# Optimization experiments

Measured on AMD Instinct MI355X. Metric: run time of the kernel, lower is better.

The kernel has to match this reference:

```python
import jax, jax.numpy as jnp
import numpy as np

B, L, D = 32, 256, 128


def hard_sigmoid(x):
    # Keras-1 default inner_activation for LSTM gates
    return jnp.clip(0.2 * x + 0.5, 0.0, 1.0)


def lstm_step(x_t, h, c, W, U, b):
    # Keras-1 gate order: i, f, c(candidate), o
    z = x_t @ W + h @ U + b  # [B, 4D]
    d = h.shape[-1]
    i = hard_sigmoid(z[:, :d])
    f = hard_sigmoid(z[:, d:2 * d])
    g = jnp.tanh(z[:, 2 * d:3 * d])
    o = hard_sigmoid(z[:, 3 * d:])
    c_new = f * c + i * g
    h_new = o * jnp.tanh(c_new)
    return h_new, c_new


def setup_inputs() -> dict:
    key = jax.random.key(0)
    ks = jax.random.split(key, 9)
    s = 0.05  # weight scale to keep activations in a sane range
    return {
        "x": jax.random.normal(ks[0], (B, L, D), dtype=jnp.float32),
        "Wr": jax.random.normal(ks[1], (D, 4 * D), dtype=jnp.float32) * s,
        "Ur": jax.random.normal(ks[2], (D, 4 * D), dtype=jnp.float32) * s,
        "br": jnp.zeros((4 * D,), dtype=jnp.float32),
        "Ww": jax.random.normal(ks[3], (D, 4 * D), dtype=jnp.float32) * s,
        "Uw": jax.random.normal(ks[4], (D, 4 * D), dtype=jnp.float32) * s,
        "bw": jnp.zeros((4 * D,), dtype=jnp.float32),
        "Wc": jax.random.normal(ks[5], (2 * D, D), dtype=jnp.float32) * s,
        "bc": jnp.zeros((D,), dtype=jnp.float32),
    }


def reference(x, Wr, Ur, br, Ww, Uw, bw, Wc, bc):
    b, l, d = x.shape
    h0 = jnp.zeros((b, d), dtype=x.dtype)

    # ---- reader LSTM (return_sequences) ----
    def reader_step(carry, x_t):
        h, c = carry
        h, c = lstm_step(x_t, h, c, Wr, Ur, br)
        return (h, c), h

    _, o_seq = jax.lax.scan(reader_step, (h0, h0), jnp.swapaxes(x, 0, 1))  # [L, B, D]

    # ---- compose-and-write scan over timesteps ----
    mem0 = x  # read() sets mem_0 = input

    def write_step(carry, o_t):
        mem, h, c = carry  # mem: [B, L, D]
        # eq 2-3: attention over memory slots
        z = jax.nn.softmax(jnp.einsum('bd,bld->bl', o_t, mem), axis=-1)  # [B, L]
        m_rt = jnp.einsum('bl,bld->bd', z, mem)  # [B, D]
        # eq 4: composer (linear activation)
        c_t = jnp.concatenate([o_t, m_rt], axis=-1) @ Wc + bc  # [B, D]
        # eq 5: writer LSTM step
        h, c = lstm_step(c_t, h, c, Ww, Uw, bw)
        # eq 6: soft overwrite of memory
        zc = z[:, :, None]
        mem = mem * (1.0 - zc) + h[:, None, :] * zc
        return (mem, h, c), h

    (_, _, _), hs = jax.lax.scan(write_step, (mem0, h0, h0), o_seq)
    # return_mode == 'last_output'
    return hs[-1]
```

## Files before the change

### kernel.cpp

```cpp
#include <hip/hip_runtime.h>
#include <stdint.h>


#define LL 256

typedef float v2f __attribute__((ext_vector_type(2)));

__device__ __forceinline__ float hsig(float x) { return fminf(fmaxf(fmaf(x, 0.2f, 0.5f), 0.f), 1.f); }
__device__ __forceinline__ float tanh_fast(float x) {
  x = fminf(fmaxf(x, -15.f), 15.f);
  float e = __expf(2.f * x);
  return (e - 1.f) / (e + 1.f);
}

__global__ __launch_bounds__(512) void wtrans_kernel(const float* __restrict__ src,
                                                     float* __restrict__ dst, int jshift) {
  int idx = blockIdx.x * 512 + threadIdx.x;
  int J = 1 << jshift;
  int k = idx >> jshift, j = idx & (J - 1);
  dst[(((size_t)(k >> 2) << jshift) + j) * 4 + (k & 3)] = src[idx];
}

__global__ __launch_bounds__(512) void pvw_gemm(const float* __restrict__ Wc,
                                                const float* __restrict__ Ww,
                                                float* __restrict__ PVw) {
  __shared__ float wrow[128];
  const int r = blockIdx.x, j = threadIdx.x;
  if (j < 128) wrow[j] = Wc[r * 128 + j];
  __syncthreads();
  float a = 0.f;
#pragma unroll 4
  for (int m = 0; m < 128; m++) a = fmaf(wrow[m], Ww[m * 512 + j], a);
  PVw[r * 512 + j] = a;
}

__global__ __launch_bounds__(512) void pz_kernel(const float* __restrict__ bc,
                                                 const float* __restrict__ Ww,
                                                 const float* __restrict__ bw,
                                                 float* __restrict__ pz) {
  __shared__ float b_s[128];
  const int j = threadIdx.x;
  if (j < 128) b_s[j] = bc[j];
  __syncthreads();
  float a = bw[j];
#pragma unroll 4
  for (int m = 0; m < 128; m++) a = fmaf(b_s[m], Ww[m * 512 + j], a);
  pz[j] = a;
}

__global__ __launch_bounds__(512) void xw_gemm(const float* __restrict__ x,
                                               const float4* __restrict__ WrT4,
                                               const float* __restrict__ br,
                                               float* __restrict__ XW) {
  alignas(16) __shared__ float xs[8][128];
  const int b = blockIdx.x >> 5, tg = blockIdx.x & 31, tid = threadIdx.x;
  const float* xg = x + ((size_t)b * LL + tg * 8) * 128;
  if (tid < 256) ((float4*)&xs[0][0])[tid] = ((const float4*)xg)[tid];
  __syncthreads();
  float acc[8];
#pragma unroll
  for (int r = 0; r < 8; r++) acc[r] = 0.f;
#pragma unroll 8
  for (int i4 = 0; i4 < 32; i4++) {
    float4 w4 = WrT4[i4 * 512 + tid];
#pragma unroll
    for (int r = 0; r < 8; r++) {
      float4 v = *(const float4*)&xs[r][4 * i4];
      acc[r] += w4.x * v.x + w4.y * v.y + w4.z * v.z + w4.w * v.w;
    }
  }
  const float brj = br[tid];
  float* o = XW + ((size_t)b * LL + tg * 8) * 512;
#pragma unroll
  for (int r = 0; r < 8; r++) o[r * 512 + tid] = acc[r] + brj;
}

__global__ __launch_bounds__(512, 2) void reader_kernel(const float4* __restrict__ UrT4,
                                                        const float* __restrict__ XW,
                                                        float* __restrict__ og) {
  alignas(16) __shared__ float h_s[128];
  alignas(16) __shared__ float pp_s[512];
  const int b = blockIdx.x, tid = threadIdx.x;
  const float* XWb = XW + (size_t)b * LL * 512;
  float* ogb = og + (size_t)b * LL * 128;

  float4 U[32];
#pragma unroll
  for (int i4 = 0; i4 < 32; i4++) U[i4] = UrT4[i4 * 512 + tid];

  float c_r = 0.f;
  if (tid < 128) h_s[tid] = 0.f;
  float xwv = XWb[tid];
  __syncthreads();

  for (int t = 0; t < LL; t++) {
    float xw_n = (t + 1 < LL) ? XWb[(t + 1) * 512 + tid] : 0.f;
    v2f acc[4] = {{0.f, 0.f}, {0.f, 0.f}, {0.f, 0.f}, {0.f, 0.f}};
#pragma unroll
    for (int i4 = 0; i4 < 32; i4++) {
      float4 v = *(const float4*)&h_s[4 * i4];
      float4 w = U[i4];
      acc[i4 & 3] += (v2f){w.x, w.y} * (v2f){v.x, v.y};
      acc[i4 & 3] += (v2f){w.z, w.w} * (v2f){v.z, v.w};
    }
    v2f A = (acc[0] + acc[1]) + (acc[2] + acc[3]);
    pp_s[tid] = A.x + A.y + xwv;
    __syncthreads();
    if (tid < 128) {
      float zi = pp_s[tid], zf = pp_s[128 + tid], zg = pp_s[256 + tid], zo = pp_s[384 + tid];
      float ii = hsig(zi), ff = hsig(zf), gg = tanh_fast(zg), oo = hsig(zo);
      c_r = fmaf(ff, c_r, ii * gg);
      float h = oo * tanh_fast(c_r);
      h_s[tid] = h;
      ogb[t * 128 + tid] = h;
    }
    __syncthreads();
    xwv = xw_n;
  }
}

__global__ __launch_bounds__(512, 2) void writer_kernel(
    const float* __restrict__ x,
    const float4* __restrict__ VwT4, const float4* __restrict__ UwT4,
    const float* __restrict__ og, const float* __restrict__ ZW,
    float* __restrict__ out, const int NC) {
  alignas(16) __shared__ float h_s[128];
  alignas(16) __shared__ float osN[128];
  alignas(16) __shared__ float sc_s[256], ee_s[256];
  alignas(16) __shared__ float mr_s[128];
  alignas(16) __shared__ float pp_s[1024];
  __shared__ float rr_s[16];
  extern __shared__ float4 UwL[];

  const int b = blockIdx.x, tid = threadIdx.x;
  const int lane = tid & 63, wv = tid >> 6;
  const int l = tid >> 1, hf = tid & 1;
  const int q = tid >> 6, dp = tid & 63;

  const float* xg = x + (size_t)b * (LL * 128);
  const float* ogb = og + (size_t)b * (LL * 128);
  const float* ZWb = ZW + (size_t)b * (LL * 512);

  for (int i = tid; i < NC * 512; i += 512) UwL[i] = UwT4[i];

  v2f Mr[32], Mc[32];
#pragma unroll
  for (int w = 0; w < 32; w++) Mr[w] = *(const v2f*)(xg + l * 128 + hf * 64 + 2 * w);
#pragma unroll
  for (int i = 0; i < 32; i++) Mc[i] = *(const v2f*)(xg + (q * 32 + i) * 128 + 2 * dp);

  float c_w = 0.f;
  if (tid < 128) { h_s[tid] = 0.f; osN[tid] = ogb[tid]; }
  __syncthreads();
  {
    v2f S = {0.f, 0.f};
#pragma unroll
    for (int w = 0; w < 32; w++) S += Mr[w] * (*(const v2f*)&osN[hf * 64 + 2 * w]);
    float s = S.x + S.y;
    s += __shfl_xor(s, 1);
    if (hf == 0) sc_s[l] = s;
  }
  __syncthreads();

  for (int t = 0; t < LL; t++) {
    float zwv = ZWb[(size_t)t * 512 + tid];
    if (tid >= 128 && tid < 256 && t + 1 < LL)
      osN[tid - 128] = ogb[(t + 1) * 128 + (tid - 128)];
    if (tid < 256) {
      float m = sc_s[tid];
#pragma unroll
      for (int off = 32; off > 0; off >>= 1) m = fmaxf(m, __shfl_xor(m, off));
      if (lane == 0) rr_s[wv] = m;
    }
    __syncthreads();
    if (tid < 256) {
      float mx = fmaxf(fmaxf(rr_s[0], rr_s[1]), fmaxf(rr_s[2], rr_s[3]));
      float e = __expf(sc_s[tid] - mx);
      ee_s[tid] = e;
      float s2 = e;
#pragma unroll
      for (int off = 32; off > 0; off >>= 1) s2 += __shfl_xor(s2, off);
      if (lane == 0) rr_s[8 + wv] = s2;
    }
    __syncthreads();
    const float inv = 1.f / (rr_s[8] + rr_s[9] + rr_s[10] + rr_s[11]);
    {
      v2f P = {0.f, 0.f};
#pragma unroll
      for (int i = 0; i < 32; i++) P += Mc[i] * ee_s[q * 32 + i];
      *(v2f*)&pp_s[q * 128 + 2 * dp] = P;
    }
    __syncthreads();
    if (tid < 128) {
      float s = 0.f;
#pragma unroll
      for (int g = 0; g < 8; g++) s += pp_s[g * 128 + tid];
      mr_s[tid] = s * inv;
    }
    __syncthreads();
    {
      v2f a0 = {0.f, 0.f}, a1 = {0.f, 0.f}, a2 = {0.f, 0.f}, a3 = {0.f, 0.f};
#pragma unroll 2
      for (int i4 = 0; i4 < 32; i4 += 2) {
        float4 w0 = VwT4[i4 * 512 + tid];
        float4 w1 = VwT4[(i4 + 1) * 512 + tid];
        float4 v0 = *(const float4*)&mr_s[4 * i4];
        float4 v1 = *(const float4*)&mr_s[4 * i4 + 4];
        a0 += (v2f){w0.x, w0.y} * (v2f){v0.x, v0.y};
        a0 += (v2f){w0.z, w0.w} * (v2f){v0.z, v0.w};
        a1 += (v2f){w1.x, w1.y} * (v2f){v1.x, v1.y};
        a1 += (v2f){w1.z, w1.w} * (v2f){v1.z, v1.w};
      }
#pragma unroll 2
      for (int i4 = 0; i4 < NC; i4 += 2) {
        float4 w0 = UwL[i4 * 512 + tid];
        float4 w1 = UwL[(i4 + 1) * 512 + tid];
        float4 v0 = *(const float4*)&h_s[4 * i4];
        float4 v1 = *(const float4*)&h_s[4 * i4 + 4];
        a2 += (v2f){w0.x, w0.y} * (v2f){v0.x, v0.y};
        a2 += (v2f){w0.z, w0.w} * (v2f){v0.z, v0.w};
        a3 += (v2f){w1.x, w1.y} * (v2f){v1.x, v1.y};
        a3 += (v2f){w1.z, w1.w} * (v2f){v1.z, v1.w};
      }
#pragma unroll 2
      for (int i4 = NC; i4 < 32; i4 += 2) {
        float4 w0 = UwT4[i4 * 512 + tid];
        float4 w1 = UwT4[(i4 + 1) * 512 + tid];
        float4 v0 = *(const float4*)&h_s[4 * i4];
        float4 v1 = *(const float4*)&h_s[4 * i4 + 4];
        a0 += (v2f){w0.x, w0.y} * (v2f){v0.x, v0.y};
        a0 += (v2f){w0.z, w0.w} * (v2f){v0.z, v0.w};
        a1 += (v2f){w1.x, w1.y} * (v2f){v1.x, v1.y};
        a1 += (v2f){w1.z, w1.w} * (v2f){v1.z, v1.w};
      }
      v2f A = (a0 + a2) + (a1 + a3);
      pp_s[tid] = A.x + A.y + zwv;
    }
    __syncthreads();
    if (tid < 128) {
      float zi = pp_s[tid], zf = pp_s[128 + tid], zg = pp_s[256 + tid], zo = pp_s[384 + tid];
      float ii = hsig(zi), ff = hsig(zf), gg = tanh_fast(zg), oo = hsig(zo);
      c_w = fmaf(ff, c_w, ii * gg);
      h_s[tid] = oo * tanh_fast(c_w);
    }
    __syncthreads();
    if (t + 1 < LL) {
      const float zr = ee_s[l] * inv;
      v2f S = {0.f, 0.f};
#pragma unroll
      for (int w = 0; w < 32; w++) {
        v2f h2 = *(const v2f*)&h_s[hf * 64 + 2 * w];
        v2f m = Mr[w];
        v2f n = m + (h2 - m) * zr;
        Mr[w] = n;
        S += n * (*(const v2f*)&osN[hf * 64 + 2 * w]);
      }
      float s = S.x + S.y;
      s += __shfl_xor(s, 1);
      if (hf == 0) sc_s[l] = s;
      v2f hc = *(const v2f*)&h_s[2 * dp];
#pragma unroll
      for (int i = 0; i < 32; i++) {
        float zc = ee_s[q * 32 + i] * inv;
        v2f m = Mc[i];
        Mc[i] = m + (hc - m) * zc;
      }
    }
    __syncthreads();
  }

  if (tid < 128) out[b * 128 + tid] = h_s[tid];
}

extern "C" void kernel_launch(void* const* d_in, const int* in_sizes, int n_in,
                              void* d_out, int out_size, void* d_ws, size_t ws_size,
                              hipStream_t stream) {
  const float* x  = (const float*)d_in[0];
  const float* Wr = (const float*)d_in[1];
  const float* Ur = (const float*)d_in[2];
  const float* br = (const float*)d_in[3];
  const float* Ww = (const float*)d_in[4];
  const float* Uw = (const float*)d_in[5];
  const float* bw = (const float*)d_in[6];
  const float* Wc = (const float*)d_in[7];
  const float* bc = (const float*)d_in[8];
  float* out = (float*)d_out;

  float* og  = (float*)d_ws;
  float* XW  = og + 1048576;
  float* WrT = XW + 4194304;
  float* UrT = WrT + 65536;
  float* UwT = UrT + 65536;
  float* PVw = UwT + 65536;
  float* PwT = PVw + 131072;
  float* VwT = PwT + 65536;
  float* pz  = VwT + 65536;

  static int nc_cached = -1;
  if (nc_cached < 0) {
    int want = 18 * 512 * (int)sizeof(float4);
    nc_cached = (hipFuncSetAttribute((const void*)writer_kernel,
                                     hipFuncAttributeMaxDynamicSharedMemorySize,
                                     want) == hipSuccess)
                    ? 18
                    : 6;
  }
  const int NC = nc_cached;
  const size_t shbytes = (size_t)NC * 512 * sizeof(float4);

  wtrans_kernel<<<128, 512, 0, stream>>>(Wr, WrT, 9);
  wtrans_kernel<<<128, 512, 0, stream>>>(Ur, UrT, 9);
  wtrans_kernel<<<128, 512, 0, stream>>>(Uw, UwT, 9);
  pvw_gemm<<<256, 512, 0, stream>>>(Wc, Ww, PVw);
  pz_kernel<<<1, 512, 0, stream>>>(bc, Ww, bw, pz);
  wtrans_kernel<<<128, 512, 0, stream>>>(PVw, PwT, 9);
  wtrans_kernel<<<128, 512, 0, stream>>>(PVw + 65536, VwT, 9);
  xw_gemm<<<1024, 512, 0, stream>>>(x, (const float4*)WrT, br, XW);
  reader_kernel<<<32, 512, 0, stream>>>((const float4*)UrT, XW, og);
  xw_gemm<<<1024, 512, 0, stream>>>(og, (const float4*)PwT, pz, XW);
  writer_kernel<<<32, 512, shbytes, stream>>>(x, (const float4*)VwT,
                                              (const float4*)UwT, og, XW, out, NC);
}
```

Measured before the change: 1.905 ms.

## Hoist writer U·h matvec before softmax and cache half of Vw in registers

The recurrent U_w·h product depends only on the previous step's h, so it now runs at the top of each timestep, ahead of the attention softmax and readout. This takes it off the serial path after the memory read. Half of the Vw weights (16 float4 per thread) are preloaded into registers so that part no longer needs a global load every step. NC becomes a template parameter so its loops have compile-time bounds. The extra 64 registers per thread, on top of the large Mr/Mc arrays, may cause spills under the 512-thread, 2-block launch bound.

```diff
diff --git a/kernel.cpp b/kernel.cpp
--- a/kernel.cpp
+++ b/kernel.cpp
@@ -119,11 +119,12 @@
   }
 }
 
+template <int NC>
 __global__ __launch_bounds__(512, 2) void writer_kernel(
     const float* __restrict__ x,
     const float4* __restrict__ VwT4, const float4* __restrict__ UwT4,
     const float* __restrict__ og, const float* __restrict__ ZW,
-    float* __restrict__ out, const int NC) {
+    float* __restrict__ out) {
   alignas(16) __shared__ float h_s[128];
   alignas(16) __shared__ float osN[128];
   alignas(16) __shared__ float sc_s[256], ee_s[256];
@@ -143,6 +144,10 @@
 
   for (int i = tid; i < NC * 512; i += 512) UwL[i] = UwT4[i];
 
+  float4 VR[16];
+#pragma unroll
+  for (int i4 = 0; i4 < 16; i4++) VR[i4] = VwT4[i4 * 512 + tid];
+
   v2f Mr[32], Mc[32];
 #pragma unroll
   for (int w = 0; w < 32; w++) Mr[w] = *(const v2f*)(xg + l * 128 + hf * 64 + 2 * w);
@@ -163,7 +168,35 @@
   __syncthreads();
 
   for (int t = 0; t < LL; t++) {
-    float zwv = ZWb[(size_t)t * 512 + tid];
+    float huv;
+    {
+      float zwv = ZWb[(size_t)t * 512 + tid];
+      v2f u0 = {0.f, 0.f}, u1 = {0.f, 0.f};
+#pragma unroll 2
+      for (int i4 = NC; i4 < 32; i4 += 2) {
+        float4 w0 = UwT4[i4 * 512 + tid];
+        float4 w1 = UwT4[(i4 + 1) * 512 + tid];
+        float4 v0 = *(const float4*)&h_s[4 * i4];
+        float4 v1 = *(const float4*)&h_s[4 * i4 + 4];
+        u0 += (v2f){w0.x, w0.y} * (v2f){v0.x, v0.y};
+        u0 += (v2f){w0.z, w0.w} * (v2f){v0.z, v0.w};
+        u1 += (v2f){w1.x, w1.y} * (v2f){v1.x, v1.y};
+        u1 += (v2f){w1.z, w1.w} * (v2f){v1.z, v1.w};
+      }
+#pragma unroll 2
+      for (int i4 = 0; i4 < NC; i4 += 2) {
+        float4 w0 = UwL[i4 * 512 + tid];
+        float4 w1 = UwL[(i4 + 1) * 512 + tid];
+        float4 v0 = *(const float4*)&h_s[4 * i4];
+        float4 v1 = *(const float4*)&h_s[4 * i4 + 4];
+        u0 += (v2f){w0.x, w0.y} * (v2f){v0.x, v0.y};
+        u0 += (v2f){w0.z, w0.w} * (v2f){v0.z, v0.w};
+        u1 += (v2f){w1.x, w1.y} * (v2f){v1.x, v1.y};
+        u1 += (v2f){w1.z, w1.w} * (v2f){v1.z, v1.w};
+      }
+      v2f U = u0 + u1;
+      huv = U.x + U.y + zwv;
+    }
     if (tid >= 128 && tid < 256 && t + 1 < LL)
       osN[tid - 128] = ogb[(t + 1) * 128 + (tid - 128)];
     if (tid < 256) {
@@ -201,7 +234,7 @@
     {
       v2f a0 = {0.f, 0.f}, a1 = {0.f, 0.f}, a2 = {0.f, 0.f}, a3 = {0.f, 0.f};
 #pragma unroll 2
-      for (int i4 = 0; i4 < 32; i4 += 2) {
+      for (int i4 = 16; i4 < 32; i4 += 2) {
         float4 w0 = VwT4[i4 * 512 + tid];
         float4 w1 = VwT4[(i4 + 1) * 512 + tid];
         float4 v0 = *(const float4*)&mr_s[4 * i4];
@@ -211,30 +244,19 @@
         a1 += (v2f){w1.x, w1.y} * (v2f){v1.x, v1.y};
         a1 += (v2f){w1.z, w1.w} * (v2f){v1.z, v1.w};
       }
-#pragma unroll 2
-      for (int i4 = 0; i4 < NC; i4 += 2) {
-        float4 w0 = UwL[i4 * 512 + tid];
-        float4 w1 = UwL[(i4 + 1) * 512 + tid];
-        float4 v0 = *(const float4*)&h_s[4 * i4];
-        float4 v1 = *(const float4*)&h_s[4 * i4 + 4];
+#pragma unroll
+      for (int i4 = 0; i4 < 16; i4 += 2) {
+        float4 w0 = VR[i4];
+        float4 w1 = VR[i4 + 1];
+        float4 v0 = *(const float4*)&mr_s[4 * i4];
+        float4 v1 = *(const float4*)&mr_s[4 * i4 + 4];
         a2 += (v2f){w0.x, w0.y} * (v2f){v0.x, v0.y};
         a2 += (v2f){w0.z, w0.w} * (v2f){v0.z, v0.w};
         a3 += (v2f){w1.x, w1.y} * (v2f){v1.x, v1.y};
         a3 += (v2f){w1.z, w1.w} * (v2f){v1.z, v1.w};
       }
-#pragma unroll 2
-      for (int i4 = NC; i4 < 32; i4 += 2) {
-        float4 w0 = UwT4[i4 * 512 + tid];
-        float4 w1 = UwT4[(i4 + 1) * 512 + tid];
-        float4 v0 = *(const float4*)&h_s[4 * i4];
-        float4 v1 = *(const float4*)&h_s[4 * i4 + 4];
-        a0 += (v2f){w0.x, w0.y} * (v2f){v0.x, v0.y};
-        a0 += (v2f){w0.z, w0.w} * (v2f){v0.z, v0.w};
-        a1 += (v2f){w1.x, w1.y} * (v2f){v1.x, v1.y};
-        a1 += (v2f){w1.z, w1.w} * (v2f){v1.z, v1.w};
-      }
       v2f A = (a0 + a2) + (a1 + a3);
-      pp_s[tid] = A.x + A.y + zwv;
+      pp_s[tid] = A.x + A.y + huv;
     }
     __syncthreads();
     if (tid < 128) {
@@ -299,14 +321,12 @@
   static int nc_cached = -1;
   if (nc_cached < 0) {
     int want = 18 * 512 * (int)sizeof(float4);
-    nc_cached = (hipFuncSetAttribute((const void*)writer_kernel,
-                                     hipFuncAttributeMaxDynamicSharedMemorySize,
-                                     want) == hipSuccess)
+    nc_cached = (hipFuncSetAttribute(
+                     reinterpret_cast<const void*>(&writer_kernel<18>),
+                     hipFuncAttributeMaxDynamicSharedMemorySize, want) == hipSuccess)
                     ? 18
                     : 6;
   }
-  const int NC = nc_cached;
-  const size_t shbytes = (size_t)NC * 512 * sizeof(float4);
 
   wtrans_kernel<<<128, 512, 0, stream>>>(Wr, WrT, 9);
   wtrans_kernel<<<128, 512, 0, stream>>>(Ur, UrT, 9);
@@ -318,6 +338,11 @@
   xw_gemm<<<1024, 512, 0, stream>>>(x, (const float4*)WrT, br, XW);
   reader_kernel<<<32, 512, 0, stream>>>((const float4*)UrT, XW, og);
   xw_gemm<<<1024, 512, 0, stream>>>(og, (const float4*)PwT, pz, XW);
-  writer_kernel<<<32, 512, shbytes, stream>>>(x, (const float4*)VwT,
-                                              (const float4*)UwT, og, XW, out, NC);
-}
+  if (nc_cached == 18) {
+    writer_kernel<18><<<32, 512, 18 * 512 * sizeof(float4), stream>>>(
+        x, (const float4*)VwT, (const float4*)UwT, og, XW, out);
+  } else {
+    writer_kernel<6><<<32, 512, 6 * 512 * sizeof(float4), stream>>>(
+        x, (const float4*)VwT, (const float4*)UwT, og, XW, out);
+  }
+}
```

Result: no change. 1.880 ms, median of 2 (-1.3%).
